# Kernel tuning notes

Measured on AMD Instinct MI355X. Metric: run time of the kernel, lower is better.

The kernel has to match this reference:

```python
import jax, jax.numpy as jnp
import numpy as np

N = 50000       # nodes
E = 1600000     # edges (avg degree 32)
D_IN = 128
HID = 64
HEADS = 2
D_OUT = 64
SLOPE = 0.2     # PyG GATConv default negative_slope


def setup_inputs() -> dict:
    key = jax.random.key(0)
    ks = jax.random.split(key, 10)
    s_in = 1.0 / np.sqrt(D_IN)
    s_h = 1.0 / np.sqrt(HEADS * HID)
    return {
        "x": jax.random.normal(ks[0], (N, D_IN), jnp.float32),
        "edge_index": jax.random.randint(ks[1], (2, E), 0, N, dtype=jnp.int64),
        "W1": jax.random.normal(ks[2], (D_IN, HEADS * HID), jnp.float32) * s_in,
        "att_src1": jax.random.normal(ks[3], (HEADS, HID), jnp.float32) * 0.1,
        "att_dst1": jax.random.normal(ks[4], (HEADS, HID), jnp.float32) * 0.1,
        "b1": jnp.zeros((HEADS * HID,), jnp.float32),
        "W2": jax.random.normal(ks[5], (HEADS * HID, D_OUT), jnp.float32) * s_h,
        "att_src2": jax.random.normal(ks[6], (1, D_OUT), jnp.float32) * 0.1,
        "att_dst2": jax.random.normal(ks[7], (1, D_OUT), jnp.float32) * 0.1,
        "b2": jnp.zeros((D_OUT,), jnp.float32),
    }


def gat_conv(x, W, a_src, a_dst, b, src, dst, num_nodes):
    """PyG GATConv (shared src/dst linear, self-loops already in src/dst), concat heads."""
    H, C = a_src.shape
    xp = (x @ W).reshape(num_nodes, H, C)          # [N,H,C]
    a_s = jnp.einsum('nhc,hc->nh', xp, a_src)       # [N,H]
    a_d = jnp.einsum('nhc,hc->nh', xp, a_dst)
    alpha = jax.nn.leaky_relu(a_s[src] + a_d[dst], SLOPE)          # [Etot,H]
    # numerically stable softmax over each destination neighborhood
    m = jax.ops.segment_max(alpha, dst, num_segments=num_nodes)     # [N,H]
    e = jnp.exp(alpha - m[dst])
    z = jax.ops.segment_sum(e, dst, num_segments=num_nodes)         # [N,H]
    coef = e / z[dst]                                               # [Etot,H]
    out = jax.ops.segment_sum(coef[:, :, None] * xp[src], dst, num_segments=num_nodes)  # [N,H,C]
    return out.reshape(num_nodes, H * C) + b


def reference(x, edge_index, W1, att_src1, att_dst1, b1, W2, att_src2, att_dst2, b2):
    loops = jnp.arange(N, dtype=edge_index.dtype)
    src = jnp.concatenate([edge_index[0], loops])   # add self-loops (PyG default)
    dst = jnp.concatenate([edge_index[1], loops])
    h = jax.nn.relu(gat_conv(x, W1, att_src1, att_dst1, b1, src, dst, N))
    return gat_conv(h, W2, att_src2, att_dst2, b2, src, dst, N)
```

## Files before the change

kernel.cpp:

```cpp
#include <hip/hip_runtime.h>
#include <hip/hip_bf16.h>
#include <hip/hip_fp16.h>


#define SLOPE 0.2f
static __device__ __forceinline__ float lrelu(float a) { return a > 0.f ? a : SLOPE * a; }

#define NBK_MAX 256

typedef _Float16 half8 __attribute__((ext_vector_type(8)));
typedef float f32x4 __attribute__((ext_vector_type(4)));


template <int CHUNK>
__global__ void bin_kernel(const int* __restrict__ src, const int* __restrict__ dst,
                           const int* __restrict__ bucket_count, int* __restrict__ bucket_cursor,
                           unsigned int* __restrict__ binned, int E, int nbk) {
  constexpr int PT = CHUNK / 256;
  __shared__ int hist[NBK_MAX];
  __shared__ int lbase[NBK_MAX];
  __shared__ int lcur[NBK_MAX];
  __shared__ int gpos[NBK_MAX];
  __shared__ unsigned int stage[CHUNK];
  __shared__ int sh[256];
  int t = threadIdx.x;
  int e0 = blockIdx.x * CHUNK;
  int cnt = min(CHUNK, E - e0);

  for (int i = t; i < nbk; i += 256) hist[i] = 0;
  __syncthreads();

  unsigned int pk[PT];
#pragma unroll
  for (int i = 0; i < PT; i++) {
    int e = e0 + t + i * 256;
    if (e < E) {
      int s = src[e], d = dst[e];
      int b = d >> 8;
      pk[i] = ((unsigned)b << 24) | ((unsigned)s << 8) | (unsigned)(d & 255);
      atomicAdd(&hist[b], 1);
    } else {
      pk[i] = 0xFFFFFFFFu;
    }
  }
  __syncthreads();

  int hv = (t < nbk) ? hist[t] : 0;
  sh[t] = hv;
  __syncthreads();
  for (int o = 1; o < 256; o <<= 1) {
    int u = (t >= o) ? sh[t - o] : 0;
    __syncthreads();
    sh[t] += u;
    __syncthreads();
  }
  if (t < nbk) {
    lbase[t] = sh[t] - hv;
    lcur[t] = sh[t] - hv;
  }
  __syncthreads();

  int gv = (t < nbk) ? bucket_count[t] : 0;
  sh[t] = gv;
  __syncthreads();
  for (int o = 1; o < 256; o <<= 1) {
    int u = (t >= o) ? sh[t - o] : 0;
    __syncthreads();
    sh[t] += u;
    __syncthreads();
  }
  if (t < nbk) {
    int gbase = sh[t] - gv;
    gpos[t] = hv ? (gbase + atomicAdd(&bucket_cursor[t], hv)) : 0;
  }
  __syncthreads();

#pragma unroll
  for (int i = 0; i < PT; i++) {
    if (pk[i] != 0xFFFFFFFFu) {
      int b = pk[i] >> 24;
      int lp = atomicAdd(&lcur[b], 1);
      stage[lp] = pk[i];
    }
  }
  __syncthreads();

  for (int i = t; i < cnt; i += 256) {
    unsigned int v = stage[i];
    int b = v >> 24;
    binned[gpos[b] + (i - lbase[b])] = v;
  }
}

template <int CAP>
__global__ void build_kernel(const unsigned int* __restrict__ binned,
                             const int* __restrict__ bucket_count, int* __restrict__ offsets,
                             int* __restrict__ csr_src, int Nn, int Etot, int nbk) {
  __shared__ int nhist[256];
  __shared__ int sh[256];
  __shared__ int lcur[256];
  __shared__ int sbase, ssz;
  __shared__ unsigned short stage[CAP];
  int b = blockIdx.x;
  int t = threadIdx.x;

  int gv = (t < nbk) ? bucket_count[t] : 0;
  sh[t] = gv;
  __syncthreads();
  for (int o = 1; o < 256; o <<= 1) {
    int u = (t >= o) ? sh[t - o] : 0;
    __syncthreads();
    sh[t] += u;
    __syncthreads();
  }
  if (t == b) { sbase = sh[t] - gv; ssz = gv; }
  __syncthreads();
  int base = sbase;
  int sz = ssz;

  nhist[t] = 0;
  __syncthreads();
  for (int i = t; i < sz; i += 256) atomicAdd(&nhist[binned[base + i] & 255], 1);
  __syncthreads();

  int hv = nhist[t];
  sh[t] = hv;
  __syncthreads();
  for (int o = 1; o < 256; o <<= 1) {
    int u = (t >= o) ? sh[t - o] : 0;
    __syncthreads();
    sh[t] += u;
    __syncthreads();
  }
  int excl = sh[t] - hv;
  int node = (b << 8) + t;
  if (node < Nn) offsets[node] = base + excl;
  if (b == nbk - 1 && t == 0) offsets[Nn] = Etot;
  lcur[t] = excl;
  __syncthreads();

  if (sz <= CAP) {
    for (int i = t; i < sz; i += 256) {
      unsigned int v = binned[base + i];
      int lp = atomicAdd(&lcur[v & 255], 1);
      stage[lp] = (unsigned short)((v >> 8) & 0xFFFFu);
    }
    __syncthreads();
    for (int i = t; i < sz; i += 256) csr_src[base + i] = (int)stage[i];
  } else {
    for (int i = t; i < sz; i += 256) {
      unsigned int v = binned[base + i];
      int lp = atomicAdd(&lcur[v & 255], 1);
      csr_src[base + lp] = (int)((v >> 8) & 0xFFFFu);
    }
  }
}


template <int K, int NOUT, int H, bool FUSE_HIST, typename AT>
__global__ __launch_bounds__(256) void gemm_att_mfma(
    const AT* __restrict__ A, const float* __restrict__ Wg,
    const float* __restrict__ att_s, const float* __restrict__ att_d,
    __half* __restrict__ Y, float* __restrict__ AS, float* __restrict__ AD, int M,
    int gemmBlocks, const int* __restrict__ dstArr, int* __restrict__ bcount,
    int E2, int histBlocks, int nbk) {
  constexpr int KK = K / 32;
  constexpr int NT = NOUT / 16;
  constexpr int NTH = NT / H;
  constexpr int LDW = K + 8;
  constexpr int LDY = NOUT + 8;
  __shared__ __half wts[NOUT * LDW];
  __shared__ __half ylds[4][16 * LDY];
  __shared__ int hh[NBK_MAX];

  int tid = threadIdx.x;

  if (FUSE_HIST && (int)blockIdx.x >= gemmBlocks) {
    int hb = blockIdx.x - gemmBlocks;
    for (int i = tid; i < nbk; i += 256) hh[i] = 0;
    __syncthreads();
    int stride = histBlocks * 256;
    for (int e = hb * 256 + tid; e < E2; e += stride)
      atomicAdd(&hh[dstArr[e] >> 8], 1);
    __syncthreads();
    for (int i = tid; i < nbk; i += 256)
      if (hh[i]) atomicAdd(&bcount[i], hh[i]);
    return;
  }

  int w = tid >> 6;
  int lane = tid & 63;
  int lrow = lane & 15;
  int lch = lane >> 4;
  int r0w = blockIdx.x * 64 + w * 16;
  bool active = (r0w < M);

  for (int idx = tid; idx < NOUT * K; idx += 256) {
    int k = idx / NOUT, c = idx - k * NOUT;
    wts[c * LDW + k] = __float2half(Wg[idx]);
  }
  __syncthreads();

  f32x4 acc[NT];
#pragma unroll
  for (int nt = 0; nt < NT; nt++) acc[nt] = (f32x4){0.f, 0.f, 0.f, 0.f};

  if (active) {
    half8 afrag[KK];
    if constexpr (sizeof(AT) == 4) {
      const float* arow = (const float*)A + (size_t)(r0w + lrow) * K + lch * 8;
#pragma unroll
      for (int kk = 0; kk < KK; kk++) {
        float4 v0 = *(const float4*)(arow + kk * 32);
        float4 v1 = *(const float4*)(arow + kk * 32 + 4);
        half8 a;
        a[0] = (_Float16)v0.x; a[1] = (_Float16)v0.y;
        a[2] = (_Float16)v0.z; a[3] = (_Float16)v0.w;
        a[4] = (_Float16)v1.x; a[5] = (_Float16)v1.y;
        a[6] = (_Float16)v1.z; a[7] = (_Float16)v1.w;
        afrag[kk] = a;
      }
    } else {
      const __half* arow = (const __half*)A + (size_t)(r0w + lrow) * K + lch * 8;
#pragma unroll
      for (int kk = 0; kk < KK; kk++) afrag[kk] = *(const half8*)(arow + kk * 32);
    }

#pragma unroll
    for (int kk = 0; kk < KK; kk++) {
#pragma unroll
      for (int nt = 0; nt < NT; nt++) {
        half8 b = *(const half8*)&wts[(nt * 16 + lrow) * LDW + kk * 32 + lch * 8];
        acc[nt] = __builtin_amdgcn_mfma_f32_16x16x32_f16(afrag[kk], b, acc[nt], 0, 0, 0);
      }
    }

    float asw[NT], adw[NT];
#pragma unroll
    for (int nt = 0; nt < NT; nt++) {
      asw[nt] = att_s[nt * 16 + lrow];
      adw[nt] = att_d[nt * 16 + lrow];
    }
#pragma unroll
    for (int h = 0; h < H; h++) {
#pragma unroll
      for (int reg = 0; reg < 4; reg++) {
        float ps = 0.f, pd = 0.f;
#pragma unroll
        for (int nt = h * NTH; nt < (h + 1) * NTH; nt++) {
          ps = fmaf(acc[nt][reg], asw[nt], ps);
          pd = fmaf(acc[nt][reg], adw[nt], pd);
        }
#pragma unroll
        for (int o = 1; o < 16; o <<= 1) {
          ps += __shfl_xor(ps, o);
          pd += __shfl_xor(pd, o);
        }
        if (lrow == 0) {
          int row = r0w + lch * 4 + reg;
          AS[row * H + h] = ps;
          AD[row * H + h] = pd;
        }
      }
    }

#pragma unroll
    for (int nt = 0; nt < NT; nt++) {
#pragma unroll
      for (int reg = 0; reg < 4; reg++) {
        ylds[w][(lch * 4 + reg) * LDY + nt * 16 + lrow] = __float2half(acc[nt][reg]);
      }
    }
  }
  __syncthreads();

  if (active) {
    constexpr int YCH = NOUT / 8;
    for (int idx = lane; idx < 16 * YCH; idx += 64) {
      int row = idx / YCH, ch = idx % YCH;
      uint4 v = *(const uint4*)&ylds[w][row * LDY + ch * 8];
      *(uint4*)(Y + (size_t)(r0w + row) * NOUT + ch * 8) = v;
    }
  }
}


static __device__ __forceinline__ void fma8(uint4 u, float e, float* __restrict__ acc) {
  float2 f0 = __half22float2(*(const __half2*)&u.x);
  float2 f1 = __half22float2(*(((const __half2*)&u.x) + 1));
  float2 f2 = __half22float2(*(const __half2*)&u.z);
  float2 f3 = __half22float2(*(((const __half2*)&u.z) + 1));
  acc[0] = fmaf(e, f0.x, acc[0]); acc[1] = fmaf(e, f0.y, acc[1]);
  acc[2] = fmaf(e, f1.x, acc[2]); acc[3] = fmaf(e, f1.y, acc[3]);
  acc[4] = fmaf(e, f2.x, acc[4]); acc[5] = fmaf(e, f2.y, acc[5]);
  acc[6] = fmaf(e, f3.x, acc[6]); acc[7] = fmaf(e, f3.y, acc[7]);
}

static __device__ __forceinline__ void pk4(uint4 u, unsigned ep, __half2* __restrict__ acc2) {
  __half2 e2 = *(const __half2*)&ep;
  acc2[0] = __hfma2(e2, *(const __half2*)&u.x, acc2[0]);
  acc2[1] = __hfma2(e2, *(((const __half2*)&u.x) + 1), acc2[1]);
  acc2[2] = __hfma2(e2, *(const __half2*)&u.z, acc2[2]);
  acc2[3] = __hfma2(e2, *(((const __half2*)&u.z) + 1), acc2[3]);
}

template <int H, bool RELU, typename OT>
__global__ void node_kernel(const int* __restrict__ offsets, const int* __restrict__ csr_src,
                            const float* __restrict__ AS, const float* __restrict__ AD,
                            const __half* __restrict__ XPH, const float* __restrict__ bias,
                            OT* __restrict__ OUT, int Nn) {
  constexpr int ROWH = H * 64;
  constexpr int LPE = (H == 2) ? 16 : 8;
  constexpr int G = 64 / LPE;
  int n = blockIdx.x;
  int lane = threadIdx.x & 63;
  int g = lane / LPE;
  int sub = lane & (LPE - 1);

  int beg = offsets[n], end = offsets[n + 1];
  int deg = end - beg;

  const __half* base = XPH + sub * 8;

  float acc[8];
#pragma unroll
  for (int k = 0; k < 8; k++) acc[k] = 0.f;
  float z0 = 0.f, z1 = 0.f;

  float ad0, ad1 = 0.f;
  if constexpr (H == 2) {
    float2 adn = ((const float2*)AD)[n];
    ad0 = adn.x; ad1 = adn.y;
  } else {
    ad0 = AD[n];
  }

  if constexpr (H == 2) {
    float2 asn = ((const float2*)AS)[n];
    float es0 = __expf(lrelu(asn.x + ad0));
    float es1 = __expf(lrelu(asn.y + ad1));
    if (g == 0) {
      uint4 u = *(const uint4*)(base + (size_t)n * ROWH);
      fma8(u, (lane & 8) ? es1 : es0, acc);
    }
    if (lane == 0) { z0 = es0; z1 = es1; }
  } else {
    float es = __expf(lrelu(AS[n] + ad0));
    if (g == 0) {
      uint4 u = *(const uint4*)(base + (size_t)n * ROWH);
      fma8(u, es, acc);
    }
    if (lane == 0) z0 = es;
  }

  for (int i0 = 0; i0 < deg; i0 += 64) {
    int cnt = min(64, deg - i0);
    int srcv = 0;
    int epk = 0;
    float ev0 = 0.f, ev1 = 0.f;
    if (lane < cnt) {
      srcv = csr_src[beg + i0 + lane];
      if constexpr (H == 2) {
        float2 asv = ((const float2*)AS)[srcv];
        ev0 = __expf(lrelu(asv.x + ad0));
        ev1 = __expf(lrelu(asv.y + ad1));
        __half h0 = __float2half(ev0), h1 = __float2half(ev1);
        epk = (int)(((unsigned)*(unsigned short*)&h1 << 16) | *(unsigned short*)&h0);
      } else {
        ev0 = __expf(lrelu(AS[srcv] + ad0));
        __half h0 = __float2half(ev0);
        unsigned short us = *(unsigned short*)&h0;
        epk = (int)(((unsigned)us << 16) | us);
      }
    }
    z0 += ev0;
    if constexpr (H == 2) z1 += ev1;

    auto sel = [&](int p) -> unsigned {
      unsigned short us;
      if constexpr (H == 2)
        us = (lane & 8) ? (unsigned short)((unsigned)p >> 16) : (unsigned short)((unsigned)p & 0xFFFFu);
      else
        us = (unsigned short)((unsigned)p & 0xFFFFu);
      return ((unsigned)us << 16) | us;
    };

    int j = 0;
    for (; j + 4 * G <= cnt; j += 4 * G) {
      int s0 = __shfl(srcv, j + g),         s1 = __shfl(srcv, j + G + g);
      int s2 = __shfl(srcv, j + 2 * G + g), s3 = __shfl(srcv, j + 3 * G + g);
      int p0 = __shfl(epk, j + g),          p1 = __shfl(epk, j + G + g);
      int p2 = __shfl(epk, j + 2 * G + g),  p3 = __shfl(epk, j + 3 * G + g);
      uint4 u0 = *(const uint4*)(base + (size_t)s0 * ROWH);
      uint4 u1 = *(const uint4*)(base + (size_t)s1 * ROWH);
      uint4 u2 = *(const uint4*)(base + (size_t)s2 * ROWH);
      uint4 u3 = *(const uint4*)(base + (size_t)s3 * ROWH);
      __half2 acc2[4];
      acc2[0] = __half2(__half(0.f), __half(0.f));
      acc2[1] = acc2[0]; acc2[2] = acc2[0]; acc2[3] = acc2[0];
      pk4(u0, sel(p0), acc2);
      pk4(u1, sel(p1), acc2);
      pk4(u2, sel(p2), acc2);
      pk4(u3, sel(p3), acc2);
#pragma unroll
      for (int k = 0; k < 4; k++) {
        float2 f = __half22float2(acc2[k]);
        acc[2 * k] += f.x;
        acc[2 * k + 1] += f.y;
      }
    }
    for (; j + G <= cnt; j += G) {
      int s = __shfl(srcv, j + g);
      int p = __shfl(epk, j + g);
      __half_raw hr; hr.x = (unsigned short)(sel(p) & 0xFFFFu);
      float e = __half2float(__half(hr));
      uint4 u = *(const uint4*)(base + (size_t)s * ROWH);
      fma8(u, e, acc);
    }
    if (j < cnt) {
      int idx = j + g;
      int s = __shfl(srcv, idx & 63);
      int p = __shfl(epk, idx & 63);
      if (idx < cnt) {
        __half_raw hr; hr.x = (unsigned short)(sel(p) & 0xFFFFu);
        float e = __half2float(__half(hr));
        uint4 u = *(const uint4*)(base + (size_t)s * ROWH);
        fma8(u, e, acc);
      }
    }
  }

#pragma unroll
  for (int o = LPE; o <= 32; o <<= 1) {
#pragma unroll
    for (int k = 0; k < 8; k++) acc[k] += __shfl_xor(acc[k], o);
  }
  for (int o = 32; o > 0; o >>= 1) {
    z0 += __shfl_xor(z0, o);
    if constexpr (H == 2) z1 += __shfl_xor(z1, o);
  }
  float inv;
  if constexpr (H == 2) inv = 1.0f / ((lane & 8) ? z1 : z0);
  else inv = 1.0f / z0;

  if (g == 0) {
    const float* bp = bias + sub * 8;
    float r[8];
#pragma unroll
    for (int k = 0; k < 8; k++) {
      r[k] = fmaf(acc[k], inv, bp[k]);
      if (RELU) r[k] = fmaxf(r[k], 0.f);
    }
    if constexpr (sizeof(OT) == 4) {
      float* op = (float*)OUT + (size_t)n * ROWH + sub * 8;
      ((float4*)op)[0] = make_float4(r[0], r[1], r[2], r[3]);
      ((float4*)op)[1] = make_float4(r[4], r[5], r[6], r[7]);
    } else {
      __half* op = (__half*)OUT + (size_t)n * ROWH + sub * 8;
      __half2 h0 = __floats2half2_rn(r[0], r[1]);
      __half2 h1 = __floats2half2_rn(r[2], r[3]);
      __half2 h2 = __floats2half2_rn(r[4], r[5]);
      __half2 h3 = __floats2half2_rn(r[6], r[7]);
      uint4 u;
      u.x = *(unsigned int*)&h0; u.y = *(unsigned int*)&h1;
      u.z = *(unsigned int*)&h2; u.w = *(unsigned int*)&h3;
      *(uint4*)op = u;
    }
  }
}


static inline size_t alignup(size_t x) { return (x + 255) & ~(size_t)255; }

extern "C" void kernel_launch(void* const* d_in, const int* in_sizes, int n_in,
                              void* d_out, int out_size, void* d_ws, size_t ws_size,
                              hipStream_t stream) {
  const float* x    = (const float*)d_in[0];
  const int*   edges= (const int*)d_in[1];
  const float* W1   = (const float*)d_in[2];
  const float* as1w = (const float*)d_in[3];
  const float* ad1w = (const float*)d_in[4];
  const float* b1   = (const float*)d_in[5];
  const float* W2   = (const float*)d_in[6];
  const float* as2w = (const float*)d_in[7];
  const float* ad2w = (const float*)d_in[8];
  const float* b2   = (const float*)d_in[9];

  const int N = in_sizes[0] / 128;
  const int E = in_sizes[1] / 2;
  const int* src = edges;
  const int* dst = edges + E;
  const int nbk = (N + 255) >> 8;

  char* p = (char*)d_ws;
  size_t off = 0;
  auto take = [&](size_t bytes) { char* r = p + off; off = alignup(off + bytes); return r; };
  __half* xph1 = (__half*)take((size_t)N * 128 * 2);
  __half* xph2 = (__half*)take((size_t)N * 64 * 2);
  __half* hbuf = (__half*)take((size_t)N * 128 * 2);
  float* as1   = (float*)take((size_t)N * 2 * 4);
  float* ad1   = (float*)take((size_t)N * 2 * 4);
  float* as2   = (float*)take((size_t)N * 4);
  float* ad2   = (float*)take((size_t)N * 4);
  int* offsets = (int*)take((size_t)(N + 1) * 4);
  int* csr_src = (int*)take((size_t)E * 4);
  unsigned int* binned = (unsigned int*)take((size_t)E * 4);
  int* bzero   = (int*)take((size_t)2 * (nbk + 1) * 4);
  int* bcount  = bzero;
  int* bcursor = bzero + (nbk + 1);
  (void)ws_size;

  constexpr int CHUNK = 2048;
  const int binBlocks = (E + CHUNK - 1) / CHUNK;
  const int gemmBlocks = (N + 63) / 64;
  const int histBlocks = 392;

  hipMemsetAsync(bzero, 0, (size_t)2 * (nbk + 1) * 4, stream);

  gemm_att_mfma<128, 128, 2, true, float><<<gemmBlocks + histBlocks, 256, 0, stream>>>(
      x, W1, as1w, ad1w, xph1, as1, ad1, N,
      gemmBlocks, dst, bcount, E, histBlocks, nbk);

  bin_kernel<CHUNK><<<binBlocks, 256, 0, stream>>>(src, dst, bcount, bcursor, binned, E, nbk);
  build_kernel<12288><<<nbk, 256, 0, stream>>>(binned, bcount, offsets, csr_src, N, E, nbk);

  node_kernel<2, true, __half><<<N, 64, 0, stream>>>(
      offsets, csr_src, as1, ad1, xph1, b1, hbuf, N);

  gemm_att_mfma<128, 64, 1, false, __half><<<gemmBlocks, 256, 0, stream>>>(
      hbuf, W2, as2w, ad2w, xph2, as2, ad2, N,
      gemmBlocks, nullptr, nullptr, 0, 0, nbk);
  node_kernel<1, false, float><<<N, 64, 0, stream>>>(
      offsets, csr_src, as2, ad2, xph2, b2, (float*)d_out, N);
}
```

Measured before the change: 170.0 us.

## Fuse edge binning into first GEMM using fixed-capacity buckets, drop histogram pass

```diff
diff --git a/kernel.cpp b/kernel.cpp
--- a/kernel.cpp
+++ b/kernel.cpp
@@ -12,181 +12,96 @@
 typedef float f32x4 __attribute__((ext_vector_type(4)));
 
 
-template <int CHUNK>
-__global__ void bin_kernel(const int* __restrict__ src, const int* __restrict__ dst,
-                           const int* __restrict__ bucket_count, int* __restrict__ bucket_cursor,
-                           unsigned int* __restrict__ binned, int E, int nbk) {
-  constexpr int PT = CHUNK / 256;
-  __shared__ int hist[NBK_MAX];
-  __shared__ int lbase[NBK_MAX];
-  __shared__ int lcur[NBK_MAX];
-  __shared__ int gpos[NBK_MAX];
-  __shared__ unsigned int stage[CHUNK];
-  __shared__ int sh[256];
-  int t = threadIdx.x;
-  int e0 = blockIdx.x * CHUNK;
-  int cnt = min(CHUNK, E - e0);
-
-  for (int i = t; i < nbk; i += 256) hist[i] = 0;
-  __syncthreads();
-
-  unsigned int pk[PT];
-#pragma unroll
-  for (int i = 0; i < PT; i++) {
-    int e = e0 + t + i * 256;
-    if (e < E) {
-      int s = src[e], d = dst[e];
-      int b = d >> 8;
-      pk[i] = ((unsigned)b << 24) | ((unsigned)s << 8) | (unsigned)(d & 255);
-      atomicAdd(&hist[b], 1);
-    } else {
-      pk[i] = 0xFFFFFFFFu;
-    }
-  }
-  __syncthreads();
-
-  int hv = (t < nbk) ? hist[t] : 0;
-  sh[t] = hv;
-  __syncthreads();
-  for (int o = 1; o < 256; o <<= 1) {
-    int u = (t >= o) ? sh[t - o] : 0;
-    __syncthreads();
-    sh[t] += u;
-    __syncthreads();
-  }
-  if (t < nbk) {
-    lbase[t] = sh[t] - hv;
-    lcur[t] = sh[t] - hv;
-  }
-  __syncthreads();
-
-  int gv = (t < nbk) ? bucket_count[t] : 0;
-  sh[t] = gv;
-  __syncthreads();
-  for (int o = 1; o < 256; o <<= 1) {
-    int u = (t >= o) ? sh[t - o] : 0;
-    __syncthreads();
-    sh[t] += u;
-    __syncthreads();
-  }
-  if (t < nbk) {
-    int gbase = sh[t] - gv;
-    gpos[t] = hv ? (gbase + atomicAdd(&bucket_cursor[t], hv)) : 0;
-  }
-  __syncthreads();
-
-#pragma unroll
-  for (int i = 0; i < PT; i++) {
-    if (pk[i] != 0xFFFFFFFFu) {
-      int b = pk[i] >> 24;
-      int lp = atomicAdd(&lcur[b], 1);
-      stage[lp] = pk[i];
-    }
-  }
-  __syncthreads();
-
-  for (int i = t; i < cnt; i += 256) {
-    unsigned int v = stage[i];
-    int b = v >> 24;
-    binned[gpos[b] + (i - lbase[b])] = v;
-  }
-}
-
-template <int CAP>
-__global__ void build_kernel(const unsigned int* __restrict__ binned,
-                             const int* __restrict__ bucket_count, int* __restrict__ offsets,
-                             int* __restrict__ csr_src, int Nn, int Etot, int nbk) {
-  __shared__ int nhist[256];
-  __shared__ int sh[256];
-  __shared__ int lcur[256];
-  __shared__ int sbase, ssz;
-  __shared__ unsigned short stage[CAP];
-  int b = blockIdx.x;
-  int t = threadIdx.x;
-
-  int gv = (t < nbk) ? bucket_count[t] : 0;
-  sh[t] = gv;
-  __syncthreads();
-  for (int o = 1; o < 256; o <<= 1) {
-    int u = (t >= o) ? sh[t - o] : 0;
-    __syncthreads();
-    sh[t] += u;
-    __syncthreads();
-  }
-  if (t == b) { sbase = sh[t] - gv; ssz = gv; }
-  __syncthreads();
-  int base = sbase;
-  int sz = ssz;
-
-  nhist[t] = 0;
-  __syncthreads();
-  for (int i = t; i < sz; i += 256) atomicAdd(&nhist[binned[base + i] & 255], 1);
-  __syncthreads();
-
-  int hv = nhist[t];
-  sh[t] = hv;
-  __syncthreads();
-  for (int o = 1; o < 256; o <<= 1) {
-    int u = (t >= o) ? sh[t - o] : 0;
-    __syncthreads();
-    sh[t] += u;
-    __syncthreads();
-  }
-  int excl = sh[t] - hv;
-  int node = (b << 8) + t;
-  if (node < Nn) offsets[node] = base + excl;
-  if (b == nbk - 1 && t == 0) offsets[Nn] = Etot;
-  lcur[t] = excl;
-  __syncthreads();
-
-  if (sz <= CAP) {
-    for (int i = t; i < sz; i += 256) {
-      unsigned int v = binned[base + i];
-      int lp = atomicAdd(&lcur[v & 255], 1);
-      stage[lp] = (unsigned short)((v >> 8) & 0xFFFFu);
-    }
-    __syncthreads();
-    for (int i = t; i < sz; i += 256) csr_src[base + i] = (int)stage[i];
-  } else {
-    for (int i = t; i < sz; i += 256) {
-      unsigned int v = binned[base + i];
-      int lp = atomicAdd(&lcur[v & 255], 1);
-      csr_src[base + lp] = (int)((v >> 8) & 0xFFFFu);
-    }
-  }
-}
-
-
-template <int K, int NOUT, int H, bool FUSE_HIST, typename AT>
-__global__ __launch_bounds__(256) void gemm_att_mfma(
+template <int K, int NOUT, int H, bool FUSE_BIN, int CHUNK, typename AT>
+__global__ __launch_bounds__(256) void gemm_bin_mfma(
     const AT* __restrict__ A, const float* __restrict__ Wg,
     const float* __restrict__ att_s, const float* __restrict__ att_d,
-    __half* __restrict__ Y, float* __restrict__ AS, float* __restrict__ AD, int M,
-    int gemmBlocks, const int* __restrict__ dstArr, int* __restrict__ bcount,
-    int E2, int histBlocks, int nbk) {
+    __half* __restrict__ Y, float* __restrict__ AS, float* __restrict__ AD,
+    int M, int gemmBlocks,
+    const int* __restrict__ srcArr, const int* __restrict__ dstArr,
+    int* __restrict__ cursor, unsigned int* __restrict__ binned,
+    int E2, int nbk, int capb) {
   constexpr int KK = K / 32;
   constexpr int NT = NOUT / 16;
   constexpr int NTH = NT / H;
   constexpr int LDW = K + 8;
   constexpr int LDY = NOUT + 8;
-  __shared__ __half wts[NOUT * LDW];
-  __shared__ __half ylds[4][16 * LDY];
-  __shared__ int hh[NBK_MAX];
+  constexpr int WTS_B = NOUT * LDW * 2;
+  constexpr int YLDS_B = 4 * 16 * LDY * 2;
+  constexpr int GEMM_B = (WTS_B > YLDS_B) ? WTS_B : YLDS_B;
+  constexpr int BIN_B = 5 * 256 * 4 + CHUNK * 4;
+  constexpr int SMEM_B = (FUSE_BIN && BIN_B > GEMM_B) ? BIN_B : GEMM_B;
+  __shared__ __align__(16) char smem[SMEM_B];
 
   int tid = threadIdx.x;
 
-  if (FUSE_HIST && (int)blockIdx.x >= gemmBlocks) {
-    int hb = blockIdx.x - gemmBlocks;
-    for (int i = tid; i < nbk; i += 256) hh[i] = 0;
-    __syncthreads();
-    int stride = histBlocks * 256;
-    for (int e = hb * 256 + tid; e < E2; e += stride)
-      atomicAdd(&hh[dstArr[e] >> 8], 1);
-    __syncthreads();
-    for (int i = tid; i < nbk; i += 256)
-      if (hh[i]) atomicAdd(&bcount[i], hh[i]);
-    return;
-  }
+  if constexpr (FUSE_BIN) {
+    if ((int)blockIdx.x >= gemmBlocks) {
+      int* hist = (int*)smem;
+      int* lbase = hist + 256;
+      int* lcur = lbase + 256;
+      int* gpos = lcur + 256;
+      int* sh = gpos + 256;
+      unsigned int* stage = (unsigned int*)(sh + 256);
+      constexpr int PT = CHUNK / 256;
+      int t = tid;
+      int bb = blockIdx.x - gemmBlocks;
+      int e0 = bb * CHUNK;
+      int cnt = min(CHUNK, E2 - e0);
+
+      hist[t] = 0;
+      __syncthreads();
+
+      unsigned int pk[PT];
+#pragma unroll
+      for (int i = 0; i < PT; i++) {
+        int e = e0 + t + i * 256;
+        if (e < E2) {
+          int s = srcArr[e], d = dstArr[e];
+          int b = d >> 8;
+          pk[i] = ((unsigned)b << 24) | ((unsigned)s << 8) | (unsigned)(d & 255);
+          atomicAdd(&hist[b], 1);
+        } else {
+          pk[i] = 0xFFFFFFFFu;
+        }
+      }
+      __syncthreads();
+
+      int hv = hist[t];
+      sh[t] = hv;
+      __syncthreads();
+      for (int o = 1; o < 256; o <<= 1) {
+        int u = (t >= o) ? sh[t - o] : 0;
+        __syncthreads();
+        sh[t] += u;
+        __syncthreads();
+      }
+      lbase[t] = sh[t] - hv;
+      lcur[t] = sh[t] - hv;
+      gpos[t] = hv ? (t * capb + atomicAdd(&cursor[t], hv)) : 0;
+      __syncthreads();
+
+#pragma unroll
+      for (int i = 0; i < PT; i++) {
+        if (pk[i] != 0xFFFFFFFFu) {
+          int b = pk[i] >> 24;
+          int lp = atomicAdd(&lcur[b], 1);
+          stage[lp] = pk[i];
+        }
+      }
+      __syncthreads();
+
+      for (int i = t; i < cnt; i += 256) {
+        unsigned int v = stage[i];
+        int b = v >> 24;
+        binned[gpos[b] + (i - lbase[b])] = v;
+      }
+      return;
+    }
+  }
+
+  __half* wts = (__half*)smem;
+  __half(*ylds)[16 * LDY] = (__half(*)[16 * LDY])smem;
 
   int w = tid >> 6;
   int lane = tid & 63;
@@ -263,7 +178,11 @@
         }
       }
     }
-
+  }
+
+  __syncthreads();
+
+  if (active) {
 #pragma unroll
     for (int nt = 0; nt < NT; nt++) {
 #pragma unroll
@@ -280,6 +199,72 @@
       int row = idx / YCH, ch = idx % YCH;
       uint4 v = *(const uint4*)&ylds[w][row * LDY + ch * 8];
       *(uint4*)(Y + (size_t)(r0w + row) * NOUT + ch * 8) = v;
+    }
+  }
+}
+
+
+template <int CAP>
+__global__ void build_kernel(const unsigned int* __restrict__ binned,
+                             const int* __restrict__ cursor, int* __restrict__ offsets,
+                             int* __restrict__ csr_src, int Nn, int Etot, int nbk, int capb) {
+  __shared__ int nhist[256];
+  __shared__ int sh[256];
+  __shared__ int lcur[256];
+  __shared__ int sbase, ssz;
+  __shared__ unsigned short stage[CAP];
+  int b = blockIdx.x;
+  int t = threadIdx.x;
+
+  int gv = (t < nbk) ? cursor[t] : 0;
+  sh[t] = gv;
+  __syncthreads();
+  for (int o = 1; o < 256; o <<= 1) {
+    int u = (t >= o) ? sh[t - o] : 0;
+    __syncthreads();
+    sh[t] += u;
+    __syncthreads();
+  }
+  if (t == b) { sbase = sh[t] - gv; ssz = gv; }
+  __syncthreads();
+  int csrbase = sbase;
+  int sz = ssz;
+  int binbase = b * capb;
+
+  nhist[t] = 0;
+  __syncthreads();
+  for (int i = t; i < sz; i += 256) atomicAdd(&nhist[binned[binbase + i] & 255], 1);
+  __syncthreads();
+
+  int hv = nhist[t];
+  sh[t] = hv;
+  __syncthreads();
+  for (int o = 1; o < 256; o <<= 1) {
+    int u = (t >= o) ? sh[t - o] : 0;
+    __syncthreads();
+    sh[t] += u;
+    __syncthreads();
+  }
+  int excl = sh[t] - hv;
+  int node = (b << 8) + t;
+  if (node < Nn) offsets[node] = csrbase + excl;
+  if (b == nbk - 1 && t == 0) offsets[Nn] = Etot;
+  lcur[t] = excl;
+  __syncthreads();
+
+  if (sz <= CAP) {
+    for (int i = t; i < sz; i += 256) {
+      unsigned int v = binned[binbase + i];
+      int lp = atomicAdd(&lcur[v & 255], 1);
+      stage[lp] = (unsigned short)((v >> 8) & 0xFFFFu);
+    }
+    __syncthreads();
+    for (int i = t; i < sz; i += 256) csr_src[csrbase + i] = (int)stage[i];
+  } else {
+    for (int i = t; i < sz; i += 256) {
+      unsigned int v = binned[binbase + i];
+      int lp = atomicAdd(&lcur[v & 255], 1);
+      csr_src[csrbase + lp] = (int)((v >> 8) & 0xFFFFu);
     }
   }
 }
@@ -492,6 +477,9 @@
   const int* dst = edges + E;
   const int nbk = (N + 255) >> 8;
 
+  constexpr int CHUNK = 2048;
+  constexpr int CAPB = 10240;
+
   char* p = (char*)d_ws;
   size_t off = 0;
   auto take = [&](size_t bytes) { char* r = p + off; off = alignup(off + bytes); return r; };
@@ -504,32 +492,27 @@
   float* ad2   = (float*)take((size_t)N * 4);
   int* offsets = (int*)take((size_t)(N + 1) * 4);
   int* csr_src = (int*)take((size_t)E * 4);
-  unsigned int* binned = (unsigned int*)take((size_t)E * 4);
-  int* bzero   = (int*)take((size_t)2 * (nbk + 1) * 4);
-  int* bcount  = bzero;
-  int* bcursor = bzero + (nbk + 1);
+  unsigned int* binned = (unsigned int*)take((size_t)nbk * CAPB * 4);
+  int* cursor  = (int*)take((size_t)NBK_MAX * 4);
   (void)ws_size;
 
-  constexpr int CHUNK = 2048;
   const int binBlocks = (E + CHUNK - 1) / CHUNK;
   const int gemmBlocks = (N + 63) / 64;
-  const int histBlocks = 392;
-
-  hipMemsetAsync(bzero, 0, (size_t)2 * (nbk + 1) * 4, stream);
-
-  gemm_att_mfma<128, 128, 2, true, float><<<gemmBlocks + histBlocks, 256, 0, stream>>>(
-      x, W1, as1w, ad1w, xph1, as1, ad1, N,
-      gemmBlocks, dst, bcount, E, histBlocks, nbk);
-
-  bin_kernel<CHUNK><<<binBlocks, 256, 0, stream>>>(src, dst, bcount, bcursor, binned, E, nbk);
-  build_kernel<12288><<<nbk, 256, 0, stream>>>(binned, bcount, offsets, csr_src, N, E, nbk);
+
+  hipMemsetAsync(cursor, 0, (size_t)NBK_MAX * 4, stream);
+
+  gemm_bin_mfma<128, 128, 2, true, CHUNK, float><<<gemmBlocks + binBlocks, 256, 0, stream>>>(
+      x, W1, as1w, ad1w, xph1, as1, ad1, N, gemmBlocks,
+      src, dst, cursor, binned, E, nbk, CAPB);
+
+  build_kernel<12288><<<nbk, 256, 0, stream>>>(binned, cursor, offsets, csr_src, N, E, nbk, CAPB);
 
   node_kernel<2, true, __half><<<N, 64, 0, stream>>>(
       offsets, csr_src, as1, ad1, xph1, b1, hbuf, N);
 
-  gemm_att_mfma<128, 64, 1, false, __half><<<gemmBlocks, 256, 0, stream>>>(
-      hbuf, W2, as2w, ad2w, xph2, as2, ad2, N,
-      gemmBlocks, nullptr, nullptr, 0, 0, nbk);
+  gemm_bin_mfma<128, 64, 1, false, CHUNK, __half><<<gemmBlocks, 256, 0, stream>>>(
+      hbuf, W2, as2w, ad2w, xph2, as2, ad2, N, gemmBlocks,
+      nullptr, nullptr, nullptr, nullptr, 0, nbk, CAPB);
   node_kernel<1, false, float><<<N, 64, 0, stream>>>(
       offsets, csr_src, as2, ad2, xph2, b2, (float*)d_out, N);
 }
```

Result: faster. 143.5 us (-15.6%).
